# Kernel optimization log

Measured on AMD Instinct MI355X. Metric: run time of the kernel, lower is better.

Reference implementation:

```python
import jax, jax.numpy as jnp
import numpy as np
import math

B, S, D, H, L, DFF = 32, 512, 1024, 16, 4, 4096
DK = D // H  # 64


def setup_inputs() -> dict:
    key = jax.random.key(0)
    ks = jax.random.split(key, 8)
    sc = 0.02
    w = lambda k, shp: (jax.random.normal(k, shp, jnp.float32) * sc)
    return dict(
        q_embed_data=jax.random.normal(ks[0], (B, S, D), jnp.float32),
        qa_embed_data=jax.random.normal(ks[1], (B, S, D), jnp.float32),
        Wk=w(ks[2], (L, D, D)), bk=jnp.zeros((L, D), jnp.float32),
        Wv=w(ks[3], (L, D, D)), bv=jnp.zeros((L, D), jnp.float32),
        Wo=w(ks[4], (L, D, D)), bo=jnp.zeros((L, D), jnp.float32),
        g1=jnp.ones((L, D), jnp.float32), be1=jnp.zeros((L, D), jnp.float32),
        W1=w(ks[5], (L, D, DFF)), c1=jnp.zeros((L, DFF), jnp.float32),
        W2=w(ks[6], (L, DFF, D)), c2=jnp.zeros((L, D), jnp.float32),
        g2=jnp.ones((L, D), jnp.float32), be2=jnp.zeros((L, D), jnp.float32),
    )


def _posemb(seqlen, d_model):
    # sinusoidal table (the 0.1*randn init is fully overwritten since d_model is even)
    pos = jnp.arange(seqlen, dtype=jnp.float32)[:, None]
    div = jnp.exp(jnp.arange(0, d_model, 2, dtype=jnp.float32) * (-math.log(10000.0) / d_model))
    pe = jnp.zeros((seqlen, d_model), jnp.float32)
    pe = pe.at[:, 0::2].set(jnp.sin(pos * div)).at[:, 1::2].set(jnp.cos(pos * div))
    return pe


def _ln(x, g, b, eps=1e-5):
    m = jnp.mean(x, axis=-1, keepdims=True)
    v = jnp.mean(jnp.square(x - m), axis=-1, keepdims=True)
    return (x - m) * jax.lax.rsqrt(v + eps) * g + b


def reference(q_embed_data, qa_embed_data, Wk, bk, Wv, bv, Wo, bo,
              g1, be1, W1, c1, W2, c2, g2, be2):
    pe = _posemb(S, D)
    x = q_embed_data + pe          # query/key stream
    y = qa_embed_data + pe         # value stream (constant across blocks)
    idx = jnp.arange(S)
    allowed = idx[:, None] > idx[None, :]  # strictly-past: triu(k=0) masked incl. diagonal

    def block(x, p):
        Wk_, bk_, Wv_, bv_, Wo_, bo_, g1_, be1_, W1_, c1_, W2_, c2_, g2_, be2_ = p
        # kq_same=1: q and k both use k_linear
        qh = (x @ Wk_ + bk_).reshape(B, S, H, DK).transpose(0, 2, 1, 3)
        kh = qh
        vh = (y @ Wv_ + bv_).reshape(B, S, H, DK).transpose(0, 2, 1, 3)
        scores = jnp.einsum('bhid,bhjd->bhij', qh, kh) / math.sqrt(DK)
        attn = jax.nn.softmax(jnp.where(allowed, scores, -1e32), axis=-1)
        # zero_pad trick: row 0 of attention is replaced by zeros
        attn = attn.at[:, :, 0, :].set(0.0)
        out = jnp.einsum('bhij,bhjd->bhid', attn, vh)
        out = out.transpose(0, 2, 1, 3).reshape(B, S, D) @ Wo_ + bo_
        x = _ln(x + out, g1_, be1_)
        ffn = jax.nn.relu(x @ W1_ + c1_) @ W2_ + c2_
        x = _ln(x + ffn, g2_, be2_)
        return x, None

    x, _ = jax.lax.scan(block, x, (Wk, bk, Wv, bv, Wo, bo, g1, be1, W1, c1, W2, c2, g2, be2))
    return x
```

## Files before the change

### kernel.cpp

```cpp
#include <hip/hip_runtime.h>


#define DEV static __device__ __forceinline__

typedef unsigned short u16;
typedef __attribute__((ext_vector_type(4))) unsigned short u16x4;
typedef __attribute__((ext_vector_type(8))) unsigned short u16x8;
typedef __attribute__((ext_vector_type(8))) short bf16x8;
typedef __attribute__((ext_vector_type(4))) float f32x4;

static constexpr int Bn = 32, Sn = 512, Dn = 1024, Hn = 16, Ln = 4, DFFn = 4096, DKn = 64;
static constexpr int Mn = Bn * Sn;

DEV u16 f2bf(float f) {
  unsigned u = __float_as_uint(f);
  u += 0x7FFFu + ((u >> 16) & 1u);
  return (u16)(u >> 16);
}
DEV float bf2f(u16 v) { return __uint_as_float((unsigned)v << 16); }

DEV void gload_lds16(const void* g, void* l) {
  __builtin_amdgcn_global_load_lds((const __attribute__((address_space(1))) void*)g,
                                   (__attribute__((address_space(3))) void*)l, 16, 0, 0);
}

DEV void barf() {
  asm volatile("" ::: "memory");
  __builtin_amdgcn_s_barrier();
  asm volatile("" ::: "memory");
}

__global__ __launch_bounds__(256) void pe_add_kernel(
    const float* __restrict__ q, const float* __restrict__ qa,
    float* __restrict__ x, u16* __restrict__ xb, u16* __restrict__ yb)
{
  size_t i4 = ((size_t)blockIdx.x * 256 + threadIdx.x) * 4;
  int d0 = (int)(i4 & (Dn - 1));
  int s  = (int)((i4 >> 10) & (Sn - 1));
  float p = (float)s;
  const float LC = 0.0089944730195f;
  float a0 = p * expf(-LC * (float)d0);
  float a2 = p * expf(-LC * (float)(d0 + 2));
  float pe0 = sinf(a0), pe1 = cosf(a0), pe2 = sinf(a2), pe3 = cosf(a2);
  const float4 qv = *(const float4*)(q + i4);
  const float4 av = *(const float4*)(qa + i4);
  float x0 = qv.x + pe0, x1 = qv.y + pe1, x2 = qv.z + pe2, x3 = qv.w + pe3;
  float y0 = av.x + pe0, y1 = av.y + pe1, y2 = av.z + pe2, y3 = av.w + pe3;
  *(float4*)(x + i4) = make_float4(x0, x1, x2, x3);
  u16x4 xv4 = { f2bf(x0), f2bf(x1), f2bf(x2), f2bf(x3) };
  u16x4 yv4 = { f2bf(y0), f2bf(y1), f2bf(y2), f2bf(y3) };
  *(u16x4*)(xb + i4) = xv4;
  *(u16x4*)(yb + i4) = yv4;
}

__global__ __launch_bounds__(256) void transpose_cast_kernel(
    const float* __restrict__ in, u16* __restrict__ out, int R, int C)
{
  __shared__ float t[32][33];
  int tx = threadIdx.x & 31, ty = threadIdx.x >> 5;
  int c0 = blockIdx.x * 32, r0 = blockIdx.y * 32;
  #pragma unroll
  for (int i = 0; i < 4; ++i)
    t[ty + i * 8][tx] = in[(size_t)(r0 + ty + i * 8) * C + c0 + tx];
  __syncthreads();
  #pragma unroll
  for (int i = 0; i < 4; ++i) {
    int rr = ty + i * 8;
    out[(size_t)(c0 + rr) * R + r0 + tx] = f2bf(t[tx][rr]);
  }
}

__global__ __launch_bounds__(256) void vtrans_kernel(const u16* __restrict__ V, u16* __restrict__ Vt)
{
  __shared__ u16 t[64][72];
  const int idx = blockIdx.x;
  const int st = idx & 7, h = (idx >> 3) & 15, b = idx >> 7;
  const int s0 = st * 64;
  const int tid = threadIdx.x;
  const int r = tid >> 3, c8 = (tid & 7) * 8;
  #pragma unroll
  for (int p = 0; p < 2; ++p) {
    int row = r + 32 * p;
    *(u16x8*)&t[row][c8] = *(const u16x8*)&V[(size_t)(b * Sn + s0 + row) * Dn + h * DKn + c8];
  }
  __syncthreads();
  #pragma unroll
  for (int p = 0; p < 2; ++p) {
    int drow = r + 32 * p;
    u16x8 w;
    #pragma unroll
    for (int j = 0; j < 8; ++j) w[j] = t[c8 + j][drow];
    *(u16x8*)&Vt[((size_t)((b * Hn + h) * DKn + drow) << 9) + s0 + c8] = w;
  }
}

template<int BIAS, int RELU, int F32OUT, int ACC>
__global__ __launch_bounds__(512, 2) void gemm8p_kernel(
    const u16* __restrict__ A, int lda,
    const u16* __restrict__ BT, int ldb,
    const float* __restrict__ bias,
    void* __restrict__ Cout, int ldc,
    int M, int N, int K)
{
  __shared__ u16 lds[2][2][16384];
  const int tid = threadIdx.x;
  const int lane = tid & 63, wid = tid >> 6;
  const int g = lane >> 4, r16 = lane & 15;
  const int wm = wid >> 2, wn = wid & 3;

  const int nwgx = N >> 8;
  const int nwg = gridDim.x * gridDim.y;
  const int flat = blockIdx.y * gridDim.x + blockIdx.x;
  const int cpx = nwg >> 3;
  const int logical = (flat & 7) * cpx + (flat >> 3);
  const int n0 = (logical % nwgx) << 8;
  const int m0 = (logical / nwgx) << 8;

  f32x4 acc[8][4];
  #pragma unroll
  for (int i = 0; i < 8; ++i)
    #pragma unroll
    for (int j = 0; j < 4; ++j) acc[i][j] = (f32x4){0.f, 0.f, 0.f, 0.f};

  const int rr = tid >> 3, ck = tid & 7;
  const int scol = ((ck ^ (rr & 7)) << 3);
  const u16* Asrc = A  + (size_t)(m0 + rr) * lda + scol;
  const u16* Bsrc = BT + (size_t)(n0 + rr) * ldb + scol;
  const int eds = rr * 64 + ck * 8;
  const size_t a64 = (size_t)64 * lda, b64 = (size_t)64 * ldb;

  #define STG(p, h, t) do {                                                  \
    if ((h) < 2) {                                                           \
      const u16* s_ = Asrc + (size_t)((h) * 128) * lda + (t) * 64;           \
      gload_lds16(s_,       &lds[p][0][eds + (h) * 8192]);                   \
      gload_lds16(s_ + a64, &lds[p][0][eds + (h) * 8192 + 4096]);            \
    } else {                                                                 \
      const u16* s_ = Bsrc + (size_t)(((h) - 2) * 128) * ldb + (t) * 64;     \
      gload_lds16(s_,       &lds[p][1][eds + ((h) - 2) * 8192]);             \
      gload_lds16(s_ + b64, &lds[p][1][eds + ((h) - 2) * 8192 + 4096]);      \
    }                                                                        \
  } while (0)

  const int c0 = ((g ^ (r16 & 7)) << 3);
  const int c1 = (((4 + g) ^ (r16 & 7)) << 3);
  const int arow = wm * 128 + r16;
  const int brow = wn * 64 + r16;

  #define LDA2(p, q, af) do {                                                        \
    af[0][0] = *(const bf16x8*)&lds[p][0][(arow + (2*(q))   * 16) * 64 + c0];        \
    af[0][1] = *(const bf16x8*)&lds[p][0][(arow + (2*(q))   * 16) * 64 + c1];        \
    af[1][0] = *(const bf16x8*)&lds[p][0][(arow + (2*(q)+1) * 16) * 64 + c0];        \
    af[1][1] = *(const bf16x8*)&lds[p][0][(arow + (2*(q)+1) * 16) * 64 + c1];        \
  } while (0)

  #define MMQ(q, af, bf) do {                                                        \
    __builtin_amdgcn_s_setprio(1);                                                   \
    _Pragma("unroll")                                                                \
    for (int ks = 0; ks < 2; ++ks)                                                   \
      _Pragma("unroll")                                                              \
      for (int i2 = 0; i2 < 2; ++i2)                                                 \
        _Pragma("unroll")                                                            \
        for (int j = 0; j < 4; ++j)                                                  \
          acc[2*(q)+i2][j] = __builtin_amdgcn_mfma_f32_16x16x32_bf16(af[i2][ks], bf[j][ks], acc[2*(q)+i2][j], 0, 0, 0); \
    __builtin_amdgcn_s_setprio(0);                                                   \
  } while (0)

  const int nt = K >> 6;
  STG(0, 0, 0); STG(0, 1, 0); STG(0, 2, 0); STG(0, 3, 0);
  if (nt > 1) {
    STG(1, 0, 1);
    asm volatile("s_waitcnt vmcnt(2)" ::: "memory");
  } else {
    asm volatile("s_waitcnt vmcnt(0)" ::: "memory");
  }
  barf();

  for (int t = 0; t < nt; ++t) {
    const int p = t & 1;
    bf16x8 bf[4][2], af[2][2];
    #pragma unroll
    for (int j = 0; j < 4; ++j) {
      bf[j][0] = *(const bf16x8*)&lds[p][1][(brow + j * 16) * 64 + c0];
      bf[j][1] = *(const bf16x8*)&lds[p][1][(brow + j * 16) * 64 + c1];
    }
    LDA2(p, 0, af);
    if (t + 1 < nt) STG(p ^ 1, 1, t + 1);
    barf();
    MMQ(0, af, bf);
    LDA2(p, 1, af);
    if (t + 1 < nt) STG(p ^ 1, 2, t + 1);
    barf();
    MMQ(1, af, bf);
    LDA2(p, 2, af);
    if (t + 1 < nt) STG(p ^ 1, 3, t + 1);
    barf();
    MMQ(2, af, bf);
    LDA2(p, 3, af);
    asm volatile("s_waitcnt lgkmcnt(0)" ::: "memory");
    barf();
    if (t + 2 < nt) STG(p, 0, t + 2);
    MMQ(3, af, bf);
    if (t + 2 < nt) {
      asm volatile("s_waitcnt vmcnt(2)" ::: "memory");
    } else {
      asm volatile("s_waitcnt vmcnt(0)" ::: "memory");
    }
    barf();
  }
  #undef STG
  #undef LDA2
  #undef MMQ

  #pragma unroll
  for (int i = 0; i < 8; ++i) {
    const int rb = m0 + wm * 128 + i * 16 + 4 * g;
    #pragma unroll
    for (int j = 0; j < 4; ++j) {
      const int col = n0 + wn * 64 + j * 16 + r16;
      float badd = BIAS ? bias[col] : 0.f;
      #pragma unroll
      for (int r = 0; r < 4; ++r) {
        size_t off = (size_t)(rb + r) * ldc + col;
        float v = acc[i][j][r] + badd;
        if (RELU) v = fmaxf(v, 0.f);
        if (F32OUT) {
          float* Cf = (float*)Cout;
          if (ACC) v += Cf[off];
          Cf[off] = v;
        } else {
          ((u16*)Cout)[off] = f2bf(v);
        }
      }
    }
  }
}

__global__ __launch_bounds__(512) void fattn_kernel(
    const u16* __restrict__ Kb, const u16* __restrict__ Vt, u16* __restrict__ O)
{
  __shared__ u16 kl[64][72];
  __shared__ u16 vl[64][72];
  __shared__ u16 pw[8][16][72];
  const int idx = blockIdx.x;
  const int qt = idx & 3;
  const int h  = (idx >> 2) & 15;
  const int b  = idx >> 6;
  const int Q0 = qt * 128;
  const int tid = threadIdx.x;
  const int lane = tid & 63, w = tid >> 6;
  const int g = lane >> 4, r16 = lane & 15;
  const int myrow = Q0 + 16 * w;

  bf16x8 qf[2];
  {
    const u16* qrow = &Kb[(size_t)(b * Sn + myrow + r16) * Dn + h * DKn];
    qf[0] = *(const bf16x8*)(qrow + 8 * g);
    qf[1] = *(const bf16x8*)(qrow + 32 + 8 * g);
  }
  f32x4 oacc[4];
  float mrow[4], lrow[4];
  #pragma unroll
  for (int j = 0; j < 4; ++j) oacc[j] = (f32x4){0.f, 0.f, 0.f, 0.f};
  #pragma unroll
  for (int r = 0; r < 4; ++r) { mrow[r] = -1e30f; lrow[r] = 0.f; }

  const int srow = tid >> 3;
  const int scol = (tid & 7) * 8;
  const u16* kbase = Kb + (size_t)(b * Sn) * Dn + h * DKn;
  const u16* vbase = Vt + (size_t)(b * Hn + h) * DKn * Sn;
  const int ctmax = 2 * qt + 1;

  for (int ct = 0; ct <= ctmax; ++ct) {
    __syncthreads();
    *(u16x8*)&kl[srow][scol] = *(const u16x8*)&kbase[(size_t)(ct * 64 + srow) * Dn + scol];
    *(u16x8*)&vl[srow][scol] = *(const u16x8*)&vbase[(size_t)srow * Sn + ct * 64 + scol];
    __syncthreads();
    if (ct * 64 > myrow + 14) continue;

    f32x4 sa[4];
    #pragma unroll
    for (int j = 0; j < 4; ++j) {
      sa[j] = (f32x4){0.f, 0.f, 0.f, 0.f};
      #pragma unroll
      for (int ks = 0; ks < 2; ++ks) {
        bf16x8 kf = *(const bf16x8*)&kl[16 * j + r16][32 * ks + 8 * g];
        sa[j] = __builtin_amdgcn_mfma_f32_16x16x32_bf16(qf[ks], kf, sa[j], 0, 0, 0);
      }
    }
    const bool needmask = (ct * 64 + 63 >= myrow);
    float p4[4][4];
    #pragma unroll
    for (int j = 0; j < 4; ++j)
      #pragma unroll
      for (int r = 0; r < 4; ++r) {
        float v = sa[j][r] * 0.125f;
        if (needmask && (ct * 64 + 16 * j + r16 >= myrow + 4 * g + r)) v = -3e38f;
        p4[j][r] = v;
      }
    #pragma unroll
    for (int r = 0; r < 4; ++r) {
      float m = fmaxf(fmaxf(p4[0][r], p4[1][r]), fmaxf(p4[2][r], p4[3][r]));
      #pragma unroll
      for (int o = 8; o; o >>= 1) m = fmaxf(m, __shfl_xor(m, o));
      float mn = fmaxf(mrow[r], m);
      float sc = __expf(mrow[r] - mn);
      mrow[r] = mn;
      float s = 0.f;
      #pragma unroll
      for (int j = 0; j < 4; ++j) {
        float e = __expf(p4[j][r] - mn);
        p4[j][r] = e;
        s += e;
      }
      #pragma unroll
      for (int o = 8; o; o >>= 1) s += __shfl_xor(s, o);
      lrow[r] = lrow[r] * sc + s;
      #pragma unroll
      for (int j = 0; j < 4; ++j) oacc[j][r] *= sc;
    }
    #pragma unroll
    for (int j = 0; j < 4; ++j)
      #pragma unroll
      for (int r = 0; r < 4; ++r)
        pw[w][4 * g + r][16 * j + r16] = f2bf(p4[j][r]);
    #pragma unroll
    for (int ks = 0; ks < 2; ++ks) {
      bf16x8 pa = *(const bf16x8*)&pw[w][r16][32 * ks + 8 * g];
      #pragma unroll
      for (int j = 0; j < 4; ++j) {
        bf16x8 vb = *(const bf16x8*)&vl[16 * j + r16][32 * ks + 8 * g];
        oacc[j] = __builtin_amdgcn_mfma_f32_16x16x32_bf16(pa, vb, oacc[j], 0, 0, 0);
      }
    }
  }
  #pragma unroll
  for (int r = 0; r < 4; ++r) {
    float inv = (lrow[r] > 0.f) ? 1.f / lrow[r] : 0.f;
    #pragma unroll
    for (int j = 0; j < 4; ++j)
      O[(size_t)(b * Sn + myrow + 4 * g + r) * Dn + h * DKn + 16 * j + r16] =
          f2bf(oacc[j][r] * inv);
  }
}

template<int TBF>
__global__ __launch_bounds__(256) void ln_kernel(
    const float* __restrict__ xin, const void* __restrict__ tin,
    const float* __restrict__ pb, const float* __restrict__ gam,
    const float* __restrict__ bet, float* __restrict__ xout, u16* __restrict__ xbout)
{
  const int row = blockIdx.x;
  const int tid = threadIdx.x;
  const size_t base = (size_t)row * Dn + tid * 4;
  float4 xv = *(const float4*)(xin + base);
  float4 tv;
  if (TBF) {
    u16x4 t4 = *(const u16x4*)((const u16*)tin + base);
    tv = make_float4(bf2f(t4[0]), bf2f(t4[1]), bf2f(t4[2]), bf2f(t4[3]));
  } else {
    tv = *(const float4*)((const float*)tin + base);
  }
  float4 bb = *(const float4*)(pb + tid * 4);
  float v0 = xv.x + tv.x + bb.x, v1 = xv.y + tv.y + bb.y;
  float v2 = xv.z + tv.z + bb.z, v3 = xv.w + tv.w + bb.w;
  float s  = v0 + v1 + v2 + v3;
  float s2 = v0 * v0 + v1 * v1 + v2 * v2 + v3 * v3;
  #pragma unroll
  for (int o = 32; o > 0; o >>= 1) { s += __shfl_xor(s, o); s2 += __shfl_xor(s2, o); }
  __shared__ float rs[4], rs2[4];
  const int wid = tid >> 6;
  if ((tid & 63) == 0) { rs[wid] = s; rs2[wid] = s2; }
  __syncthreads();
  s  = rs[0] + rs[1] + rs[2] + rs[3];
  s2 = rs2[0] + rs2[1] + rs2[2] + rs2[3];
  const float mean = s * (1.f / Dn);
  const float var  = s2 * (1.f / Dn) - mean * mean;
  const float rstd = rsqrtf(fmaxf(var, 0.f) + 1e-5f);
  float4 gv = *(const float4*)(gam + tid * 4);
  float4 bv = *(const float4*)(bet + tid * 4);
  float o0 = (v0 - mean) * rstd * gv.x + bv.x;
  float o1 = (v1 - mean) * rstd * gv.y + bv.y;
  float o2 = (v2 - mean) * rstd * gv.z + bv.z;
  float o3 = (v3 - mean) * rstd * gv.w + bv.w;
  *(float4*)(xout + base) = make_float4(o0, o1, o2, o3);
  u16x4 ub = { f2bf(o0), f2bf(o1), f2bf(o2), f2bf(o3) };
  *(u16x4*)(xbout + base) = ub;
}

extern "C" void kernel_launch(void* const* d_in, const int* in_sizes, int n_in,
                              void* d_out, int out_size, void* d_ws, size_t ws_size,
                              hipStream_t stream)
{
  const float* q   = (const float*)d_in[0];
  const float* qa  = (const float*)d_in[1];
  const float* Wk  = (const float*)d_in[2];
  const float* bk  = (const float*)d_in[3];
  const float* Wv  = (const float*)d_in[4];
  const float* bv  = (const float*)d_in[5];
  const float* Wo  = (const float*)d_in[6];
  const float* bo  = (const float*)d_in[7];
  const float* g1  = (const float*)d_in[8];
  const float* be1 = (const float*)d_in[9];
  const float* W1  = (const float*)d_in[10];
  const float* c1  = (const float*)d_in[11];
  const float* W2  = (const float*)d_in[12];
  const float* c2  = (const float*)d_in[13];
  const float* g2  = (const float*)d_in[14];
  const float* be2 = (const float*)d_in[15];
  float* x = (float*)d_out;

  const size_t MD  = (size_t)Mn * Dn;
  const size_t MF  = (size_t)Mn * DFFn;
  const size_t WSZ = 3 * (size_t)Dn * Dn * 2 + 2 * (size_t)Dn * DFFn * 2;
  const size_t NEED_SMALL = 5 * MD * 2 + WSZ + 8192;
  const size_t NEED_BIG   = 2 * MD * 2 + MF * 2 + MD * 4 + WSZ + 8192;
  if (ws_size < NEED_SMALL) return;
  const bool big = (ws_size >= NEED_BIG);

  char* wsb = (char*)d_ws;
  size_t off = 0;
  auto take = [&](size_t bytes) -> void* {
    void* r = wsb + off;
    off += (bytes + 255) & ~(size_t)255;
    return r;
  };
  u16 *XB, *YB, *KB, *VT, *VB, *H1 = nullptr;
  float* TMP;
  XB = (u16*)take(MD * 2);
  YB = (u16*)take(MD * 2);
  if (big) {
    H1  = (u16*)take(MF * 2);
    TMP = (float*)take(MD * 4);
    KB  = H1;
    VT  = H1 + MD;
    VB  = H1 + 2 * MD;
  } else {
    KB  = (u16*)take(MD * 2);
    VT  = (u16*)take(MD * 2);
    VB  = (u16*)take(MD * 2);
    TMP = (float*)KB;
  }
  u16* WKT = (u16*)take((size_t)Dn * Dn * 2);
  u16* WVT = (u16*)take((size_t)Dn * Dn * 2);
  u16* WOT = (u16*)take((size_t)Dn * Dn * 2);
  u16* W1T = (u16*)take((size_t)Dn * DFFn * 2);
  u16* W2T = (u16*)take((size_t)Dn * DFFn * 2);
  u16* H1C = VB;
  u16* TMPB = (u16*)TMP;
  (void)in_sizes; (void)n_in; (void)out_size;

  pe_add_kernel<<<Mn * Dn / 1024, 256, 0, stream>>>(q, qa, x, XB, YB);

  const dim3 g256(Dn / 256, Mn / 256);
  const dim3 gW1(DFFn / 256, Mn / 256);
  for (int l = 0; l < Ln; ++l) {
    const size_t wo = (size_t)l * Dn * Dn;
    const size_t fo = (size_t)l * Dn * DFFn;
    transpose_cast_kernel<<<dim3(32, 32), 256, 0, stream>>>(Wk + wo, WKT, Dn, Dn);
    transpose_cast_kernel<<<dim3(32, 32), 256, 0, stream>>>(Wv + wo, WVT, Dn, Dn);
    transpose_cast_kernel<<<dim3(32, 32), 256, 0, stream>>>(Wo + wo, WOT, Dn, Dn);
    transpose_cast_kernel<<<dim3(128, 32), 256, 0, stream>>>(W1 + fo, W1T, Dn, DFFn);
    transpose_cast_kernel<<<dim3(32, 128), 256, 0, stream>>>(W2 + fo, W2T, DFFn, Dn);

    gemm8p_kernel<1,0,0,0><<<g256, 512, 0, stream>>>(XB, Dn, WKT, Dn, bk + l * Dn, KB, Dn, Mn, Dn, Dn);
    gemm8p_kernel<1,0,0,0><<<g256, 512, 0, stream>>>(YB, Dn, WVT, Dn, bv + l * Dn, VB, Dn, Mn, Dn, Dn);
    vtrans_kernel<<<Bn * Hn * 8, 256, 0, stream>>>(VB, VT);
    fattn_kernel<<<Bn * Hn * 4, 512, 0, stream>>>(KB, VT, VB);
    if (big) {
      gemm8p_kernel<0,0,0,0><<<g256, 512, 0, stream>>>(VB, Dn, WOT, Dn, nullptr, TMPB, Dn, Mn, Dn, Dn);
      ln_kernel<1><<<Mn, 256, 0, stream>>>(x, TMPB, bo + l * Dn, g1 + l * Dn, be1 + l * Dn, x, XB);
      gemm8p_kernel<1,1,0,0><<<gW1, 512, 0, stream>>>(
          XB, Dn, W1T, Dn, c1 + l * DFFn, H1, DFFn, Mn, DFFn, Dn);
      gemm8p_kernel<0,0,0,0><<<g256, 512, 0, stream>>>(
          H1, DFFn, W2T, DFFn, nullptr, TMPB, Dn, Mn, Dn, DFFn);
      ln_kernel<1><<<Mn, 256, 0, stream>>>(x, TMPB, c2 + l * Dn, g2 + l * Dn, be2 + l * Dn, x, XB);
    } else {
      gemm8p_kernel<0,0,1,0><<<g256, 512, 0, stream>>>(VB, Dn, WOT, Dn, nullptr, TMP, Dn, Mn, Dn, Dn);
      ln_kernel<0><<<Mn, 256, 0, stream>>>(x, TMP, bo + l * Dn, g1 + l * Dn, be1 + l * Dn, x, XB);
      for (int ci = 0; ci < 4; ++ci) {
        gemm8p_kernel<1,1,0,0><<<g256, 512, 0, stream>>>(
            XB, Dn, W1T + (size_t)ci * Dn * Dn, Dn, c1 + l * DFFn + ci * Dn, H1C, Dn, Mn, Dn, Dn);
        if (ci == 0)
          gemm8p_kernel<0,0,1,0><<<g256, 512, 0, stream>>>(
              H1C, Dn, W2T + (size_t)ci * Dn, DFFn, nullptr, TMP, Dn, Mn, Dn, Dn);
        else
          gemm8p_kernel<0,0,1,1><<<g256, 512, 0, stream>>>(
              H1C, Dn, W2T + (size_t)ci * Dn, DFFn, nullptr, TMP, Dn, Mn, Dn, Dn);
      }
      ln_kernel<0><<<Mn, 256, 0, stream>>>(x, TMP, c2 + l * Dn, g2 + l * Dn, be2 + l * Dn, x, XB);
    }
  }
}
```

Measured before the change: 2.251 ms.

## Batch K/V projection GEMMs and weight casts, reorder GEMM prefetch stages

The Wk, Wv and Wo transpose-casts now run as one launch indexed by blockIdx.z. The K and V projection GEMMs become a single dual-problem launch, where the z-index picks the operand set. Inside the GEMM main loop, the global-to-LDS staging of the next tile is moved earlier, so stages 1 and 2 are issued together before the first MFMA group. This cuts launch overhead and tail idling between small kernels, and starts loads sooner. The cost is more in-flight memory traffic early in each iteration, and this reorder applies to every GEMM in the model.

```diff
diff --git a/kernel.cpp b/kernel.cpp
--- a/kernel.cpp
+++ b/kernel.cpp
@@ -70,6 +70,27 @@
   }
 }
 
+__global__ __launch_bounds__(256) void transpose_cast3_kernel(
+    const float* __restrict__ i0, const float* __restrict__ i1, const float* __restrict__ i2,
+    u16* __restrict__ o0, u16* __restrict__ o1, u16* __restrict__ o2)
+{
+  const int z = blockIdx.z;
+  const float* in = (z == 0) ? i0 : (z == 1) ? i1 : i2;
+  u16* out = (z == 0) ? o0 : (z == 1) ? o1 : o2;
+  __shared__ float t[32][33];
+  int tx = threadIdx.x & 31, ty = threadIdx.x >> 5;
+  int c0 = blockIdx.x * 32, r0 = blockIdx.y * 32;
+  #pragma unroll
+  for (int i = 0; i < 4; ++i)
+    t[ty + i * 8][tx] = in[(size_t)(r0 + ty + i * 8) * Dn + c0 + tx];
+  __syncthreads();
+  #pragma unroll
+  for (int i = 0; i < 4; ++i) {
+    int rr = ty + i * 8;
+    out[(size_t)(c0 + rr) * Dn + r0 + tx] = f2bf(t[tx][rr]);
+  }
+}
+
 __global__ __launch_bounds__(256) void vtrans_kernel(const u16* __restrict__ V, u16* __restrict__ Vt)
 {
   __shared__ u16 t[64][72];
@@ -94,14 +115,17 @@
   }
 }
 
-template<int BIAS, int RELU, int F32OUT, int ACC>
+template<int BIAS, int RELU, int F32OUT, int ACC, int DUAL = 0>
 __global__ __launch_bounds__(512, 2) void gemm8p_kernel(
     const u16* __restrict__ A, int lda,
     const u16* __restrict__ BT, int ldb,
     const float* __restrict__ bias,
     void* __restrict__ Cout, int ldc,
-    int M, int N, int K)
-{
+    int M, int N, int K,
+    const u16* A2 = nullptr, const u16* BT2 = nullptr,
+    const float* bias2 = nullptr, void* Cout2 = nullptr)
+{
+  if (DUAL && blockIdx.z) { A = A2; BT = BT2; bias = bias2; Cout = Cout2; }
   __shared__ u16 lds[2][2][16384];
   const int tid = threadIdx.x;
   const int lane = tid & 63, wid = tid >> 6;
@@ -184,15 +208,14 @@
       bf[j][1] = *(const bf16x8*)&lds[p][1][(brow + j * 16) * 64 + c1];
     }
     LDA2(p, 0, af);
-    if (t + 1 < nt) STG(p ^ 1, 1, t + 1);
+    if (t + 1 < nt) { STG(p ^ 1, 1, t + 1); STG(p ^ 1, 2, t + 1); }
     barf();
     MMQ(0, af, bf);
     LDA2(p, 1, af);
-    if (t + 1 < nt) STG(p ^ 1, 2, t + 1);
+    if (t + 1 < nt) STG(p ^ 1, 3, t + 1);
     barf();
     MMQ(1, af, bf);
     LDA2(p, 2, af);
-    if (t + 1 < nt) STG(p ^ 1, 3, t + 1);
     barf();
     MMQ(2, af, bf);
     LDA2(p, 3, af);
@@ -452,18 +475,19 @@
   pe_add_kernel<<<Mn * Dn / 1024, 256, 0, stream>>>(q, qa, x, XB, YB);
 
   const dim3 g256(Dn / 256, Mn / 256);
+  const dim3 g256z(Dn / 256, Mn / 256, 2);
   const dim3 gW1(DFFn / 256, Mn / 256);
   for (int l = 0; l < Ln; ++l) {
     const size_t wo = (size_t)l * Dn * Dn;
     const size_t fo = (size_t)l * Dn * DFFn;
-    transpose_cast_kernel<<<dim3(32, 32), 256, 0, stream>>>(Wk + wo, WKT, Dn, Dn);
-    transpose_cast_kernel<<<dim3(32, 32), 256, 0, stream>>>(Wv + wo, WVT, Dn, Dn);
-    transpose_cast_kernel<<<dim3(32, 32), 256, 0, stream>>>(Wo + wo, WOT, Dn, Dn);
+    transpose_cast3_kernel<<<dim3(32, 32, 3), 256, 0, stream>>>(
+        Wk + wo, Wv + wo, Wo + wo, WKT, WVT, WOT);
     transpose_cast_kernel<<<dim3(128, 32), 256, 0, stream>>>(W1 + fo, W1T, Dn, DFFn);
     transpose_cast_kernel<<<dim3(32, 128), 256, 0, stream>>>(W2 + fo, W2T, DFFn, Dn);
 
-    gemm8p_kernel<1,0,0,0><<<g256, 512, 0, stream>>>(XB, Dn, WKT, Dn, bk + l * Dn, KB, Dn, Mn, Dn, Dn);
-    gemm8p_kernel<1,0,0,0><<<g256, 512, 0, stream>>>(YB, Dn, WVT, Dn, bv + l * Dn, VB, Dn, Mn, Dn, Dn);
+    gemm8p_kernel<1,0,0,0,1><<<g256z, 512, 0, stream>>>(
+        XB, Dn, WKT, Dn, bk + l * Dn, KB, Dn, Mn, Dn, Dn,
+        YB, WVT, bv + l * Dn, VB);
     vtrans_kernel<<<Bn * Hn * 8, 256, 0, stream>>>(VB, VT);
     fattn_kernel<<<Bn * Hn * 4, 512, 0, stream>>>(KB, VT, VB);
     if (big) {
```

Result: no change. 2.218 ms (-1.5%).
